# Performance work log

Measured on AMD Instinct MI355X. Metric: run time of the kernel, lower is better.

The kernel has to match this reference:

```python
import jax, jax.numpy as jnp
import numpy as np

N_A, N_P, E = 50000, 50000, 600000
H, D = 8, 16
C = H * D  # hidden_channels = 128
OUT = 16
F_A, F_P = 256, 128
NEG_SLOPE = 0.2
EPS = 1e-5


def setup_inputs():
    key = jax.random.key(0)
    ks = jax.random.split(key, 16)
    return {
        'x_author': jax.random.normal(ks[0], (N_A, F_A), jnp.float32),
        'x_paper': jax.random.normal(ks[1], (N_P, F_P), jnp.float32),
        'W_a': jax.random.normal(ks[2], (F_A, C), jnp.float32) / np.sqrt(F_A).astype(np.float32),
        'b_a': jnp.zeros((C,), jnp.float32),
        'W_p': jax.random.normal(ks[3], (F_P, C), jnp.float32) / np.sqrt(F_P).astype(np.float32),
        'b_p': jnp.zeros((C,), jnp.float32),
        'att_src_ap': jax.random.normal(ks[4], (H, D), jnp.float32) * 0.1,
        'att_dst_ap': jax.random.normal(ks[5], (H, D), jnp.float32) * 0.1,
        'att_src_pp': jax.random.normal(ks[6], (H, D), jnp.float32) * 0.1,
        'att_dst_pp': jax.random.normal(ks[7], (H, D), jnp.float32) * 0.1,
        'k_W': jax.random.normal(ks[8], (C, C), jnp.float32) / np.sqrt(C).astype(np.float32),
        'k_b': jnp.zeros((C,), jnp.float32),
        'q': jax.random.normal(ks[9], (C,), jnp.float32) * 0.1,
        'norm_w': jnp.ones((C,), jnp.float32),
        'norm_b': jnp.zeros((C,), jnp.float32),
        'norm_ms': jnp.ones((C,), jnp.float32),
        'lin_W': jax.random.normal(ks[10], (C, OUT), jnp.float32) / np.sqrt(C).astype(np.float32),
        'lin_b': jnp.zeros((OUT,), jnp.float32),
        'edge_ap': jax.random.randint(ks[11], (2, E), 0, N_A),
        'edge_pp': jax.random.randint(ks[12], (2, E), 0, N_P),
    }


def _edge_type_out(h_src, h_dst, edge, a_src, a_dst, n_dst):
    # Node-level attention for one edge type (PyG HANConv per-metapath GAT).
    alpha_s = jnp.einsum('nhd,hd->nh', h_src, a_src)  # [N_src, H]
    alpha_d = jnp.einsum('nhd,hd->nh', h_dst, a_dst)  # [N_dst, H]
    src, dst = edge[0], edge[1]
    alpha = alpha_s[src] + alpha_d[dst]                       # [E, H]
    alpha = jnp.where(alpha >= 0, alpha, NEG_SLOPE * alpha)   # leaky_relu(0.2)
    m = jax.ops.segment_max(alpha, dst, num_segments=n_dst)
    e = jnp.exp(alpha - m[dst])
    denom = jax.ops.segment_sum(e, dst, num_segments=n_dst)
    attn = e / denom[dst]                                     # softmax over incoming edges
    msg = h_src[src] * attn[:, :, None]                       # [E, H, D]
    out = jax.ops.segment_sum(msg, dst, num_segments=n_dst)   # [n_dst, H, D]
    return jax.nn.relu(out.reshape(n_dst, H * D))


def reference(x_author, x_paper, W_a, b_a, W_p, b_p, att_src_ap, att_dst_ap,
              att_src_pp, att_dst_pp, k_W, k_b, q, norm_w, norm_b, norm_ms,
              lin_W, lin_b, edge_ap, edge_pp):
    # per-node-type projections -> [N, H, D]
    h_a = (x_author @ W_a + b_a).reshape(N_A, H, D)
    h_p = (x_paper @ W_p + b_p).reshape(N_P, H, D)
    # per-edge-type node-level attention + aggregation (both target 'paper')
    out_ap = _edge_type_out(h_a, h_p, edge_ap, att_src_ap, att_dst_ap, N_P)
    out_pp = _edge_type_out(h_p, h_p, edge_pp, att_src_pp, att_dst_pp, N_P)
    # semantic-level attention across the R=2 meta-paths
    outs = jnp.stack([out_ap, out_pp], axis=0)               # [R, N_P, C]
    w = jnp.tanh(outs @ k_W + k_b).mean(axis=1) @ q          # [R]
    beta = jax.nn.softmax(w)
    out = jnp.einsum('rnc,r->nc', outs, beta)                # [N_P, C]
    # GraphNorm (single graph: stats over all nodes)
    mean = out.mean(axis=0)
    o = out - mean * norm_ms
    var = (o * o).mean(axis=0)
    o = norm_w * o / jnp.sqrt(var + EPS) + norm_b
    # final classifier
    return o @ lin_W + lin_b
```

## Files before the change

### kernel.cpp

```cpp
#include <hip/hip_runtime.h>
#include <math.h>

#define NN   50000
#define EE   600000
#define CCH  128
#define HH   8
#define DD   16
#define OUTC 16
#define NEG  0.2f
#define EPSN 1e-5f
#define SCHUNKS 1172
#define CAP 64
#define SBKT 32

typedef _Float16 f16x8 __attribute__((ext_vector_type(8)));
typedef float    f32x4 __attribute__((ext_vector_type(4)));

__device__ __forceinline__ float fast_tanh(float x) {
    x = fminf(10.f, fmaxf(-10.f, x));
    float e = __expf(2.f * x);
    return (e - 1.f) / (e + 1.f);
}

__device__ __forceinline__ float lrelu(float x) {
    return (x >= 0.f) ? x : NEG * x;
}

__global__ __launch_bounds__(256) void convw_k(const float* __restrict__ W_a,
        const float* __restrict__ W_p, const float* __restrict__ k_W,
        const float* __restrict__ lin_W, _Float16* __restrict__ Wt_a,
        _Float16* __restrict__ Wt_p, _Float16* __restrict__ kWt,
        _Float16* __restrict__ linWt)
{
    int id = blockIdx.x * 256 + threadIdx.x;
    if (id < 32768) {
        int k = id >> 7, n = id & 127;
        Wt_a[n * 256 + k] = (_Float16)W_a[id];
    } else if (id < 49152) {
        int i = id - 32768; int k = i >> 7, n = i & 127;
        Wt_p[n * 128 + k] = (_Float16)W_p[i];
    } else if (id < 65536) {
        int i = id - 49152; int k = i >> 7, n = i & 127;
        kWt[n * 128 + k] = (_Float16)k_W[i];
    } else if (id < 67584) {
        int i = id - 65536; int k = i >> 4, n = i & 15;
        linWt[n * 128 + k] = (_Float16)lin_W[i];
    }
}

__global__ __launch_bounds__(256) void gemm2h_k(const float* __restrict__ X_a,
        const float* __restrict__ X_p, const _Float16* __restrict__ Wt_a,
        const _Float16* __restrict__ Wt_p, const float* __restrict__ b_a,
        const float* __restrict__ b_p,
        const float* __restrict__ att_s_ap, const float* __restrict__ att_d_ap,
        const float* __restrict__ att_s_pp, const float* __restrict__ att_d_pp,
        _Float16* __restrict__ h_a, _Float16* __restrict__ h_p,
        float* __restrict__ as_ap, float* __restrict__ ad_ap,
        float* __restrict__ as_pp, float* __restrict__ ad_pp,
        const int* __restrict__ ea, const int* __restrict__ ep,
        int* __restrict__ fill, int* __restrict__ csrp, int GBn)
{
    __shared__ _Float16 As[64][40];
    __shared__ _Float16 Bs[128][40];
    const int t = threadIdx.x;
    if ((int)blockIdx.x >= 2 * GBn) {
        int bb = (int)blockIdx.x - 2 * GBn;
        int base = bb * 1024 + t;
        int d[4];
#pragma unroll
        for (int it = 0; it < 4; ++it) {
            int e = base + it * 256;
            int dd = -1;
            if (e < EE) dd = ea[EE + e];
            else if (e < 2 * EE) dd = NN + ep[e];
            d[it] = dd;
        }
#pragma unroll
        for (int it = 0; it < 4; ++it) {
            int dd = d[it];
            if (dd >= 0) {
                int e = base + it * 256;
                int pos = atomicAdd(&fill[dd], 1);
                if (pos < CAP) {
                    int s = (e < EE) ? ea[e] : ep[e - EE];
                    csrp[(size_t)dd * CAP + pos] = s;
                }
            }
        }
        return;
    }
    const int which = ((int)blockIdx.x >= GBn) ? 1 : 0;
    const float* X = which ? X_p : X_a;
    const _Float16* Wt = which ? Wt_p : Wt_a;
    const float* bias = which ? b_p : b_a;
    _Float16* Y = which ? h_p : h_a;
    const int K = which ? 128 : 256;
    const int r0 = (blockIdx.x - which * GBn) * 64;
    const int lane = t & 63;
    const int wv = t >> 6;
    const int m16 = lane & 15;
    const int kq = lane >> 4;
    f32x4 acc[8];
#pragma unroll
    for (int i = 0; i < 8; ++i) acc[i] = (f32x4){0.f, 0.f, 0.f, 0.f};

    const int ar = t >> 2;
    const int ak = (t & 3) * 8;
    const int br = t >> 1;
    const int bk = (t & 1) * 16;

    for (int kc = 0; kc < K; kc += 32) {
        int row = r0 + ar;
        f16x8 av;
        if (row < NN) {
            const float4* gp = (const float4*)&X[row * K + kc + ak];
            float4 x0 = gp[0], x1 = gp[1];
            av[0] = (_Float16)x0.x; av[1] = (_Float16)x0.y;
            av[2] = (_Float16)x0.z; av[3] = (_Float16)x0.w;
            av[4] = (_Float16)x1.x; av[5] = (_Float16)x1.y;
            av[6] = (_Float16)x1.z; av[7] = (_Float16)x1.w;
        } else {
#pragma unroll
            for (int j = 0; j < 8; ++j) av[j] = (_Float16)0.f;
        }
        *(f16x8*)&As[ar][ak] = av;
        const f16x8* wp = (const f16x8*)&Wt[br * K + kc + bk];
        *(f16x8*)&Bs[br][bk]     = wp[0];
        *(f16x8*)&Bs[br][bk + 8] = wp[1];
        __syncthreads();
        f16x8 af = *(const f16x8*)&As[wv * 16 + m16][kq * 8];
#pragma unroll
        for (int i = 0; i < 8; ++i) {
            f16x8 bf = *(const f16x8*)&Bs[i * 16 + m16][kq * 8];
            acc[i] = __builtin_amdgcn_mfma_f32_16x16x32_f16(af, bf, acc[i], 0, 0, 0);
        }
        __syncthreads();
    }
    const int rbase = r0 + wv * 16 + kq * 4;
#pragma unroll
    for (int i = 0; i < 8; ++i) {
        int col = i * 16 + m16;
        float bv = bias[col];
        float hv[4];
#pragma unroll
        for (int rr = 0; rr < 4; ++rr) hv[rr] = acc[i][rr] + bv;
#pragma unroll
        for (int rr = 0; rr < 4; ++rr)
            if (rbase + rr < NN) Y[(rbase + rr) * 128 + col] = (_Float16)hv[rr];
        if (which == 0) {
            float av = att_s_ap[i * 16 + m16];
            float p[4];
#pragma unroll
            for (int rr = 0; rr < 4; ++rr) p[rr] = hv[rr] * av;
#pragma unroll
            for (int x = 1; x < 16; x <<= 1)
#pragma unroll
                for (int rr = 0; rr < 4; ++rr) p[rr] += __shfl_xor(p[rr], x, 64);
            if (m16 == 0) {
#pragma unroll
                for (int rr = 0; rr < 4; ++rr)
                    if (rbase + rr < NN) as_ap[(rbase + rr) * 8 + i] = p[rr];
            }
        } else {
            float a1 = att_d_ap[i * 16 + m16];
            float a2 = att_s_pp[i * 16 + m16];
            float a3 = att_d_pp[i * 16 + m16];
            float p1[4], p2[4], p3[4];
#pragma unroll
            for (int rr = 0; rr < 4; ++rr) {
                p1[rr] = hv[rr] * a1; p2[rr] = hv[rr] * a2; p3[rr] = hv[rr] * a3;
            }
#pragma unroll
            for (int x = 1; x < 16; x <<= 1) {
#pragma unroll
                for (int rr = 0; rr < 4; ++rr) {
                    p1[rr] += __shfl_xor(p1[rr], x, 64);
                    p2[rr] += __shfl_xor(p2[rr], x, 64);
                    p3[rr] += __shfl_xor(p3[rr], x, 64);
                }
            }
            if (m16 == 0) {
#pragma unroll
                for (int rr = 0; rr < 4; ++rr) {
                    if (rbase + rr < NN) {
                        ad_ap[(rbase + rr) * 8 + i] = p1[rr];
                        as_pp[(rbase + rr) * 8 + i] = p2[rr];
                        ad_pp[(rbase + rr) * 8 + i] = p3[rr];
                    }
                }
            }
        }
    }
}

__device__ __forceinline__ void agg_path(
        const _Float16* __restrict__ hsrc, const float* __restrict__ as,
        float adv, int cnt, const int* __restrict__ row, int h, int sub,
        float* acc, float& l)
{
    int4 r0 = *(const int4*)&row[0];
    int4 r1 = *(const int4*)&row[4];
    int4 r2 = *(const int4*)&row[8];
    int4 r3 = *(const int4*)&row[12];
    int s[16] = {r0.x, r0.y, r0.z, r0.w, r1.x, r1.y, r1.z, r1.w,
                 r2.x, r2.y, r2.z, r2.w, r3.x, r3.y, r3.z, r3.w};
#pragma unroll
    for (int e = 0; e < 16; ++e) s[e] = (e < cnt) ? s[e] : 0;
    float av[16];
#pragma unroll
    for (int e = 0; e < 16; ++e) av[e] = as[s[e] * 8 + h];
    f16x8 hv[16];
#pragma unroll
    for (int e = 0; e < 16; ++e)
        hv[e] = *(const f16x8*)&hsrc[(size_t)s[e] * CCH + sub * 8];
#pragma unroll
    for (int e = 0; e < 16; ++e) {
        float w = (e < cnt) ? __expf(lrelu(av[e] + adv)) : 0.f;
        l += w;
#pragma unroll
        for (int i = 0; i < 8; ++i) acc[i] += w * (float)hv[e][i];
    }
    if (cnt > 16) {
        int4 r4 = *(const int4*)&row[16];
        int4 r5 = *(const int4*)&row[20];
        int s2[8] = {r4.x, r4.y, r4.z, r4.w, r5.x, r5.y, r5.z, r5.w};
#pragma unroll
        for (int e = 0; e < 8; ++e) s2[e] = (16 + e < cnt) ? s2[e] : 0;
        float av2[8];
#pragma unroll
        for (int e = 0; e < 8; ++e) av2[e] = as[s2[e] * 8 + h];
        f16x8 hv2[8];
#pragma unroll
        for (int e = 0; e < 8; ++e)
            hv2[e] = *(const f16x8*)&hsrc[(size_t)s2[e] * CCH + sub * 8];
#pragma unroll
        for (int e = 0; e < 8; ++e) {
            float w = (16 + e < cnt) ? __expf(lrelu(av2[e] + adv)) : 0.f;
            l += w;
#pragma unroll
            for (int i = 0; i < 8; ++i) acc[i] += w * (float)hv2[e][i];
        }
        for (int p = 24; p < cnt; ++p) {
            int s0 = row[p];
            float w = __expf(lrelu(as[s0 * 8 + h] + adv));
            f16x8 v = *(const f16x8*)&hsrc[(size_t)s0 * CCH + sub * 8];
            l += w;
#pragma unroll
            for (int i = 0; i < 8; ++i) acc[i] += w * (float)v[i];
        }
    }
}

__global__ __launch_bounds__(256) void agg4f_k(
        const _Float16* __restrict__ h_a, const _Float16* __restrict__ h_p,
        const float* __restrict__ as_ap, const float* __restrict__ ad_ap,
        const float* __restrict__ as_pp, const float* __restrict__ ad_pp,
        const int* __restrict__ fill, const int* __restrict__ csrp,
        const _Float16* __restrict__ kWt, const float* __restrict__ kb,
        const float* __restrict__ qv,
        _Float16* __restrict__ out_ap, _Float16* __restrict__ out_pp,
        float* __restrict__ wacc, float* __restrict__ statsb)
{
    __shared__ _Float16 Aap[16][136];
    __shared__ _Float16 App[16][136];
    __shared__ float sbuf[640];
    __shared__ float wred[4];
    const int t = threadIdx.x;
    const int wave = t >> 6, lane = t & 63;
    const int q = lane >> 4, sub = lane & 15;
    const int slot = wave * 4 + q;
    const int n = blockIdx.x * 16 + slot;
    const int h = sub >> 1;
    for (int i = t; i < 640; i += 256) sbuf[i] = 0.f;

    float adva = ad_ap[n * 8 + h];
    float advp = ad_pp[n * 8 + h];
    int cnt_a = fill[n];      if (cnt_a > CAP) cnt_a = CAP;
    int cnt_p = fill[NN + n]; if (cnt_p > CAP) cnt_p = CAP;
    float la = 0.f, lp = 0.f;
    float accA[8] = {0.f,0.f,0.f,0.f,0.f,0.f,0.f,0.f};
    float accP[8] = {0.f,0.f,0.f,0.f,0.f,0.f,0.f,0.f};

    agg_path(h_a, as_ap, adva, cnt_a, &csrp[(size_t)n * CAP],        h, sub, accA, la);
    agg_path(h_p, as_pp, advp, cnt_p, &csrp[(size_t)(NN + n) * CAP], h, sub, accP, lp);

    float inva = (la > 0.f) ? 1.f/la : 0.f;
    float invp = (lp > 0.f) ? 1.f/lp : 0.f;
    float oa[8], ob[8];
#pragma unroll
    for (int i = 0; i < 8; ++i) {
        oa[i] = fmaxf(accA[i]*inva, 0.f);
        ob[i] = fmaxf(accP[i]*invp, 0.f);
    }
    f16x8 va, vb;
#pragma unroll
    for (int i = 0; i < 8; ++i) { va[i] = (_Float16)oa[i]; vb[i] = (_Float16)ob[i]; }
    *(f16x8*)&out_ap[n * CCH + sub * 8] = va;
    *(f16x8*)&out_pp[n * CCH + sub * 8] = vb;
    *(f16x8*)&Aap[slot][sub * 8] = va;
    *(f16x8*)&App[slot][sub * 8] = vb;
    float sa[8], sb[8], ssa[8], ssb[8], sab[8];
#pragma unroll
    for (int j = 0; j < 8; ++j) {
        float a = oa[j], bq = ob[j];
        sa[j] = a; sb[j] = bq; ssa[j] = a*a; ssb[j] = bq*bq; sab[j] = a*bq;
    }
#pragma unroll
    for (int x = 16; x < 64; x <<= 1) {
#pragma unroll
        for (int j = 0; j < 8; ++j) {
            sa[j]  += __shfl_xor(sa[j],  x, 64);
            sb[j]  += __shfl_xor(sb[j],  x, 64);
            ssa[j] += __shfl_xor(ssa[j], x, 64);
            ssb[j] += __shfl_xor(ssb[j], x, 64);
            sab[j] += __shfl_xor(sab[j], x, 64);
        }
    }
    __syncthreads();
    if (lane < 16) {
        int c0 = sub * 8;
#pragma unroll
        for (int j = 0; j < 8; ++j) {
            atomicAdd(&sbuf[c0 + j],       sa[j]);
            atomicAdd(&sbuf[128 + c0 + j], sb[j]);
            atomicAdd(&sbuf[256 + c0 + j], ssa[j]);
            atomicAdd(&sbuf[384 + c0 + j], ssb[j]);
            atomicAdd(&sbuf[512 + c0 + j], sab[j]);
        }
    }
    const int m16 = lane & 15, kq = lane >> 4;
    const int path = wave >> 1;
    float local = 0.f;
#pragma unroll
    for (int j = 0; j < 4; ++j) {
        int ct = (wave & 1) * 4 + j;
        f32x4 acc2 = (f32x4){0.f, 0.f, 0.f, 0.f};
#pragma unroll
        for (int kc = 0; kc < 128; kc += 32) {
            f16x8 af = path ? *(const f16x8*)&App[m16][kc + kq * 8]
                            : *(const f16x8*)&Aap[m16][kc + kq * 8];
            f16x8 bf = *(const f16x8*)&kWt[(ct * 16 + m16) * 128 + kc + kq * 8];
            acc2 = __builtin_amdgcn_mfma_f32_16x16x32_f16(af, bf, acc2, 0, 0, 0);
        }
        float kbc = kb[ct * 16 + m16], qc = qv[ct * 16 + m16];
#pragma unroll
        for (int rr = 0; rr < 4; ++rr)
            local += fast_tanh(acc2[rr] + kbc) * qc;
    }
#pragma unroll
    for (int x = 1; x < 64; x <<= 1) local += __shfl_xor(local, x, 64);
    if (lane == 0) wred[wave] = local;
    __syncthreads();
    if (t == 0) atomicAdd(&wacc[(blockIdx.x & 15) * 16],       wred[0] + wred[1]);
    if (t == 1) atomicAdd(&wacc[256 + (blockIdx.x & 15) * 16], wred[2] + wred[3]);
    if (t < 128) {
        float* sp = statsb + (size_t)(blockIdx.x & (SBKT - 1)) * 128;
        atomicAdd(&sp[t],                sbuf[t]);
        atomicAdd(&sp[SBKT*128 + t],     sbuf[128 + t]);
        atomicAdd(&sp[2*SBKT*128 + t],   sbuf[256 + t]);
        atomicAdd(&sp[3*SBKT*128 + t],   sbuf[384 + t]);
        atomicAdd(&sp[4*SBKT*128 + t],   sbuf[512 + t]);
    }
}

__global__ __launch_bounds__(256) void final2_k(
        const _Float16* __restrict__ oa, const _Float16* __restrict__ ob,
        const float* __restrict__ wacc, const float* __restrict__ statsb,
        const float* __restrict__ ms, const float* __restrict__ nw,
        const float* __restrict__ nb,
        const _Float16* __restrict__ linWt, const float* __restrict__ linb,
        float* __restrict__ out)
{
    __shared__ _Float16 As[64][136];
    __shared__ float scl[128], shf[128];
    __shared__ float bcoef[2];
    int t = threadIdx.x;
    if (t < 128) {
        float w0s = 0.f, w1s = 0.f;
#pragma unroll
        for (int i = 0; i < 16; ++i) {
            w0s += wacc[i * 16];
            w1s += wacc[256 + i * 16];
        }
        float w0 = w0s * (1.f / NN), w1 = w1s * (1.f / NN);
        float mm = fmaxf(w0, w1);
        float e0 = __expf(w0 - mm), e1 = __expf(w1 - mm);
        float b0 = e0 / (e0 + e1), b1 = e1 / (e0 + e1);
        if (t == 0) { bcoef[0] = b0; bcoef[1] = b1; }
        int c = t;
        float vsA = 0.f, vsB = 0.f, vssA = 0.f, vssB = 0.f, vsAB = 0.f;
        for (int i = 0; i < SBKT; ++i) {
            vsA  += statsb[i * 128 + c];
            vsB  += statsb[SBKT*128 + i * 128 + c];
            vssA += statsb[2*SBKT*128 + i * 128 + c];
            vssB += statsb[3*SBKT*128 + i * 128 + c];
            vsAB += statsb[4*SBKT*128 + i * 128 + c];
        }
        float mean = (b0 * vsA + b1 * vsB) * (1.f / NN);
        float ex2 = (b0 * b0 * vssA + 2.f * b0 * b1 * vsAB + b1 * b1 * vssB) * (1.f / NN);
        float a = mean * ms[c];
        float var = ex2 - 2.f * a * mean + a * a;
        float sc = nw[c] * rsqrtf(var + EPSN);
        scl[c] = sc;
        shf[c] = nb[c] - a * sc;
    }
    __syncthreads();
    float b0 = bcoef[0], b1 = bcoef[1];
    int r0 = blockIdx.x * 64;
    int row = t >> 2, cp = (t & 3) * 32;
    int gr = r0 + row;
    if (gr < NN) {
#pragma unroll
        for (int i = 0; i < 4; ++i) {
            int c0 = cp + i * 8;
            f16x8 va = *(const f16x8*)&oa[gr * CCH + c0];
            f16x8 vb = *(const f16x8*)&ob[gr * CCH + c0];
            f16x8 o;
#pragma unroll
            for (int e2 = 0; e2 < 8; ++e2) {
                float v = b0 * (float)va[e2] + b1 * (float)vb[e2];
                o[e2] = (_Float16)(v * scl[c0 + e2] + shf[c0 + e2]);
            }
            *(f16x8*)&As[row][c0] = o;
        }
    } else {
        f16x8 z;
#pragma unroll
        for (int e2 = 0; e2 < 8; ++e2) z[e2] = (_Float16)0.f;
#pragma unroll
        for (int i = 0; i < 4; ++i) *(f16x8*)&As[row][cp + i * 8] = z;
    }
    __syncthreads();
    int lane = t & 63, wv = t >> 6;
    int m16 = lane & 15, kq = lane >> 4;
    f32x4 acc = (f32x4){0.f, 0.f, 0.f, 0.f};
#pragma unroll
    for (int kc = 0; kc < 128; kc += 32) {
        f16x8 af = *(const f16x8*)&As[wv * 16 + m16][kc + kq * 8];
        f16x8 bf = *(const f16x8*)&linWt[m16 * 128 + kc + kq * 8];
        acc = __builtin_amdgcn_mfma_f32_16x16x32_f16(af, bf, acc, 0, 0, 0);
    }
    float lb = linb[m16];
#pragma unroll
    for (int r = 0; r < 4; ++r) {
        int gr2 = r0 + wv * 16 + kq * 4 + r;
        if (gr2 < NN) out[gr2 * 16 + m16] = acc[r] + lb;
    }
}

extern "C" void kernel_launch(void* const* d_in, const int* in_sizes, int n_in,
                              void* d_out, int out_size, void* d_ws, size_t ws_size,
                              hipStream_t stream) {
    const float* x_a   = (const float*)d_in[0];
    const float* x_p   = (const float*)d_in[1];
    const float* W_a   = (const float*)d_in[2];
    const float* b_a   = (const float*)d_in[3];
    const float* W_p   = (const float*)d_in[4];
    const float* b_p   = (const float*)d_in[5];
    const float* att_src_ap = (const float*)d_in[6];
    const float* att_dst_ap = (const float*)d_in[7];
    const float* att_src_pp = (const float*)d_in[8];
    const float* att_dst_pp = (const float*)d_in[9];
    const float* k_W   = (const float*)d_in[10];
    const float* k_b   = (const float*)d_in[11];
    const float* q     = (const float*)d_in[12];
    const float* norm_w = (const float*)d_in[13];
    const float* norm_b = (const float*)d_in[14];
    const float* norm_ms = (const float*)d_in[15];
    const float* lin_W = (const float*)d_in[16];
    const float* lin_b = (const float*)d_in[17];
    const int* edge_ap = (const int*)d_in[18];
    const int* edge_pp = (const int*)d_in[19];
    float* out = (float*)d_out;

    char* base = (char*)d_ws;
    size_t off = 0;
    auto alloc = [&](size_t bytes) -> void* {
        void* r = base + off;
        off += (bytes + 255) & ~(size_t)255;
        return r;
    };
    _Float16* h_a    = (_Float16*)alloc((size_t)NN * CCH * 2);
    _Float16* h_p    = (_Float16*)alloc((size_t)NN * CCH * 2);
    _Float16* out_ap = (_Float16*)alloc((size_t)NN * CCH * 2);
    _Float16* out_pp = (_Float16*)alloc((size_t)NN * CCH * 2);
    float* as_ap  = (float*)alloc((size_t)NN * HH * 4);
    float* ad_ap  = (float*)alloc((size_t)NN * HH * 4);
    float* as_pp  = (float*)alloc((size_t)NN * HH * 4);
    float* ad_pp  = (float*)alloc((size_t)NN * HH * 4);
    _Float16* Wt_a = (_Float16*)alloc((size_t)128 * 256 * 2);
    _Float16* Wt_p = (_Float16*)alloc((size_t)128 * 128 * 2);
    _Float16* kWt  = (_Float16*)alloc((size_t)128 * 128 * 2);
    _Float16* linWt = (_Float16*)alloc((size_t)16 * 128 * 2);
    int* csrp = (int*)alloc((size_t)2 * NN * CAP * 4);
    const size_t ZCOUNT = 100000 + 512 + 5 * SBKT * 128;
    int* zz = (int*)alloc(ZCOUNT * 4);
    int* fill   = zz;
    float* wacc = (float*)(zz + 100000);
    float* statsb = (float*)(zz + 100512);

    (void)in_sizes; (void)n_in; (void)out_size; (void)ws_size;

    hipMemsetAsync(zz, 0, ZCOUNT * 4, stream);

    convw_k<<<264, 256, 0, stream>>>(W_a, W_p, k_W, lin_W, Wt_a, Wt_p, kWt, linWt);

    const int GB = (NN + 63) / 64;
    gemm2h_k<<<2 * GB + SCHUNKS, 256, 0, stream>>>(
        x_a, x_p, Wt_a, Wt_p, b_a, b_p,
        att_src_ap, att_dst_ap, att_src_pp, att_dst_pp,
        h_a, h_p, as_ap, ad_ap, as_pp, ad_pp,
        edge_ap, edge_pp, fill, csrp, GB);

    agg4f_k<<<NN / 16, 256, 0, stream>>>(h_a, h_p, as_ap, ad_ap, as_pp, ad_pp,
                                         fill, csrp, kWt, k_b, q,
                                         out_ap, out_pp, wacc, statsb);

    final2_k<<<GB, 256, 0, stream>>>(out_ap, out_pp, wacc, statsb,
                                     norm_ms, norm_w, norm_b, linWt, lin_b, out);
}
```

Measured before the change: 334.0 us.

## Split aggregation waves per metapath, store attention logits in fp16, simplify stats

The aggregation kernel now gives each wave one metapath for 8 nodes per block, instead of having every wave walk both metapaths for 16 nodes. This doubles the grid and halves the serial gather work per thread, which should expose more memory-level parallelism. The per-node attention logits are stored as fp16 to cut gather bytes. GraphNorm statistics are now summed from the shared tiles by 128 threads, replacing the shuffle and shared-atomic reductions. The cost is zero-padded MFMA rows that do wasted work, fp16 rounding of the attention logits, and twice as many global atomics.

```diff
diff --git a/kernel.cpp b/kernel.cpp
--- a/kernel.cpp
+++ b/kernel.cpp
@@ -55,8 +55,8 @@
         const float* __restrict__ att_s_ap, const float* __restrict__ att_d_ap,
         const float* __restrict__ att_s_pp, const float* __restrict__ att_d_pp,
         _Float16* __restrict__ h_a, _Float16* __restrict__ h_p,
-        float* __restrict__ as_ap, float* __restrict__ ad_ap,
-        float* __restrict__ as_pp, float* __restrict__ ad_pp,
+        _Float16* __restrict__ as_ap, _Float16* __restrict__ ad_ap,
+        _Float16* __restrict__ as_pp, _Float16* __restrict__ ad_pp,
         const int* __restrict__ ea, const int* __restrict__ ep,
         int* __restrict__ fill, int* __restrict__ csrp, int GBn)
 {
@@ -159,7 +159,7 @@
             if (m16 == 0) {
 #pragma unroll
                 for (int rr = 0; rr < 4; ++rr)
-                    if (rbase + rr < NN) as_ap[(rbase + rr) * 8 + i] = p[rr];
+                    if (rbase + rr < NN) as_ap[(rbase + rr) * 8 + i] = (_Float16)p[rr];
             }
         } else {
             float a1 = att_d_ap[i * 16 + m16];
@@ -183,9 +183,9 @@
 #pragma unroll
                 for (int rr = 0; rr < 4; ++rr) {
                     if (rbase + rr < NN) {
-                        ad_ap[(rbase + rr) * 8 + i] = p1[rr];
-                        as_pp[(rbase + rr) * 8 + i] = p2[rr];
-                        ad_pp[(rbase + rr) * 8 + i] = p3[rr];
+                        ad_ap[(rbase + rr) * 8 + i] = (_Float16)p1[rr];
+                        as_pp[(rbase + rr) * 8 + i] = (_Float16)p2[rr];
+                        ad_pp[(rbase + rr) * 8 + i] = (_Float16)p3[rr];
                     }
                 }
             }
@@ -194,7 +194,7 @@
 }
 
 __device__ __forceinline__ void agg_path(
-        const _Float16* __restrict__ hsrc, const float* __restrict__ as,
+        const _Float16* __restrict__ hsrc, const _Float16* __restrict__ as,
         float adv, int cnt, const int* __restrict__ row, int h, int sub,
         float* acc, float& l)
 {
@@ -208,7 +208,7 @@
     for (int e = 0; e < 16; ++e) s[e] = (e < cnt) ? s[e] : 0;
     float av[16];
 #pragma unroll
-    for (int e = 0; e < 16; ++e) av[e] = as[s[e] * 8 + h];
+    for (int e = 0; e < 16; ++e) av[e] = (float)as[s[e] * 8 + h];
     f16x8 hv[16];
 #pragma unroll
     for (int e = 0; e < 16; ++e)
@@ -228,7 +228,7 @@
         for (int e = 0; e < 8; ++e) s2[e] = (16 + e < cnt) ? s2[e] : 0;
         float av2[8];
 #pragma unroll
-        for (int e = 0; e < 8; ++e) av2[e] = as[s2[e] * 8 + h];
+        for (int e = 0; e < 8; ++e) av2[e] = (float)as[s2[e] * 8 + h];
         f16x8 hv2[8];
 #pragma unroll
         for (int e = 0; e < 8; ++e)
@@ -242,7 +242,7 @@
         }
         for (int p = 24; p < cnt; ++p) {
             int s0 = row[p];
-            float w = __expf(lrelu(as[s0 * 8 + h] + adv));
+            float w = __expf(lrelu((float)as[s0 * 8 + h] + adv));
             f16x8 v = *(const f16x8*)&hsrc[(size_t)s0 * CCH + sub * 8];
             l += w;
 #pragma unroll
@@ -253,8 +253,8 @@
 
 __global__ __launch_bounds__(256) void agg4f_k(
         const _Float16* __restrict__ h_a, const _Float16* __restrict__ h_p,
-        const float* __restrict__ as_ap, const float* __restrict__ ad_ap,
-        const float* __restrict__ as_pp, const float* __restrict__ ad_pp,
+        const _Float16* __restrict__ as_ap, const _Float16* __restrict__ ad_ap,
+        const _Float16* __restrict__ as_pp, const _Float16* __restrict__ ad_pp,
         const int* __restrict__ fill, const int* __restrict__ csrp,
         const _Float16* __restrict__ kWt, const float* __restrict__ kb,
         const float* __restrict__ qv,
@@ -263,73 +263,46 @@
 {
     __shared__ _Float16 Aap[16][136];
     __shared__ _Float16 App[16][136];
-    __shared__ float sbuf[640];
     __shared__ float wred[4];
     const int t = threadIdx.x;
     const int wave = t >> 6, lane = t & 63;
     const int q = lane >> 4, sub = lane & 15;
-    const int slot = wave * 4 + q;
-    const int n = blockIdx.x * 16 + slot;
+    const int pw = wave >> 1;
+    const int slot = (wave & 1) * 4 + q;
+    const int n = blockIdx.x * 8 + slot;
     const int h = sub >> 1;
-    for (int i = t; i < 640; i += 256) sbuf[i] = 0.f;
-
-    float adva = ad_ap[n * 8 + h];
-    float advp = ad_pp[n * 8 + h];
-    int cnt_a = fill[n];      if (cnt_a > CAP) cnt_a = CAP;
-    int cnt_p = fill[NN + n]; if (cnt_p > CAP) cnt_p = CAP;
-    float la = 0.f, lp = 0.f;
-    float accA[8] = {0.f,0.f,0.f,0.f,0.f,0.f,0.f,0.f};
-    float accP[8] = {0.f,0.f,0.f,0.f,0.f,0.f,0.f,0.f};
-
-    agg_path(h_a, as_ap, adva, cnt_a, &csrp[(size_t)n * CAP],        h, sub, accA, la);
-    agg_path(h_p, as_pp, advp, cnt_p, &csrp[(size_t)(NN + n) * CAP], h, sub, accP, lp);
-
-    float inva = (la > 0.f) ? 1.f/la : 0.f;
-    float invp = (lp > 0.f) ? 1.f/lp : 0.f;
-    float oa[8], ob[8];
-#pragma unroll
-    for (int i = 0; i < 8; ++i) {
-        oa[i] = fmaxf(accA[i]*inva, 0.f);
-        ob[i] = fmaxf(accP[i]*invp, 0.f);
-    }
-    f16x8 va, vb;
-#pragma unroll
-    for (int i = 0; i < 8; ++i) { va[i] = (_Float16)oa[i]; vb[i] = (_Float16)ob[i]; }
-    *(f16x8*)&out_ap[n * CCH + sub * 8] = va;
-    *(f16x8*)&out_pp[n * CCH + sub * 8] = vb;
-    *(f16x8*)&Aap[slot][sub * 8] = va;
-    *(f16x8*)&App[slot][sub * 8] = vb;
-    float sa[8], sb[8], ssa[8], ssb[8], sab[8];
-#pragma unroll
-    for (int j = 0; j < 8; ++j) {
-        float a = oa[j], bq = ob[j];
-        sa[j] = a; sb[j] = bq; ssa[j] = a*a; ssb[j] = bq*bq; sab[j] = a*bq;
-    }
-#pragma unroll
-    for (int x = 16; x < 64; x <<= 1) {
-#pragma unroll
-        for (int j = 0; j < 8; ++j) {
-            sa[j]  += __shfl_xor(sa[j],  x, 64);
-            sb[j]  += __shfl_xor(sb[j],  x, 64);
-            ssa[j] += __shfl_xor(ssa[j], x, 64);
-            ssb[j] += __shfl_xor(ssb[j], x, 64);
-            sab[j] += __shfl_xor(sab[j], x, 64);
-        }
+    {
+        _Float16* za = &Aap[8][0];
+        _Float16* zb = &App[8][0];
+        for (int i = t; i < 8 * 136; i += 256) {
+            za[i] = (_Float16)0.f; zb[i] = (_Float16)0.f;
+        }
+    }
+    const _Float16* hsrc = pw ? h_p : h_a;
+    const _Float16* as   = pw ? as_pp : as_ap;
+    const _Float16* ad   = pw ? ad_pp : ad_ap;
+    const int gnode = pw ? NN + n : n;
+    float adv = (float)ad[n * 8 + h];
+    int cnt = fill[gnode]; if (cnt > CAP) cnt = CAP;
+    const int* row = &csrp[(size_t)gnode * CAP];
+    float l = 0.f;
+    float acc[8] = {0.f,0.f,0.f,0.f,0.f,0.f,0.f,0.f};
+
+    agg_path(hsrc, as, adv, cnt, row, h, sub, acc, l);
+
+    float inv = (l > 0.f) ? 1.f / l : 0.f;
+    f16x8 vo;
+#pragma unroll
+    for (int i = 0; i < 8; ++i) vo[i] = (_Float16)fmaxf(acc[i] * inv, 0.f);
+    if (pw == 0) {
+        *(f16x8*)&out_ap[n * CCH + sub * 8] = vo;
+        *(f16x8*)&Aap[slot][sub * 8] = vo;
+    } else {
+        *(f16x8*)&out_pp[n * CCH + sub * 8] = vo;
+        *(f16x8*)&App[slot][sub * 8] = vo;
     }
     __syncthreads();
-    if (lane < 16) {
-        int c0 = sub * 8;
-#pragma unroll
-        for (int j = 0; j < 8; ++j) {
-            atomicAdd(&sbuf[c0 + j],       sa[j]);
-            atomicAdd(&sbuf[128 + c0 + j], sb[j]);
-            atomicAdd(&sbuf[256 + c0 + j], ssa[j]);
-            atomicAdd(&sbuf[384 + c0 + j], ssb[j]);
-            atomicAdd(&sbuf[512 + c0 + j], sab[j]);
-        }
-    }
     const int m16 = lane & 15, kq = lane >> 4;
-    const int path = wave >> 1;
     float local = 0.f;
 #pragma unroll
     for (int j = 0; j < 4; ++j) {
@@ -337,15 +310,17 @@
         f32x4 acc2 = (f32x4){0.f, 0.f, 0.f, 0.f};
 #pragma unroll
         for (int kc = 0; kc < 128; kc += 32) {
-            f16x8 af = path ? *(const f16x8*)&App[m16][kc + kq * 8]
-                            : *(const f16x8*)&Aap[m16][kc + kq * 8];
+            f16x8 af = pw ? *(const f16x8*)&App[m16][kc + kq * 8]
+                          : *(const f16x8*)&Aap[m16][kc + kq * 8];
             f16x8 bf = *(const f16x8*)&kWt[(ct * 16 + m16) * 128 + kc + kq * 8];
             acc2 = __builtin_amdgcn_mfma_f32_16x16x32_f16(af, bf, acc2, 0, 0, 0);
         }
-        float kbc = kb[ct * 16 + m16], qc = qv[ct * 16 + m16];
-#pragma unroll
-        for (int rr = 0; rr < 4; ++rr)
-            local += fast_tanh(acc2[rr] + kbc) * qc;
+        if (kq < 2) {
+            float kbc = kb[ct * 16 + m16], qc = qv[ct * 16 + m16];
+#pragma unroll
+            for (int rr = 0; rr < 4; ++rr)
+                local += fast_tanh(acc2[rr] + kbc) * qc;
+        }
     }
 #pragma unroll
     for (int x = 1; x < 64; x <<= 1) local += __shfl_xor(local, x, 64);
@@ -354,12 +329,20 @@
     if (t == 0) atomicAdd(&wacc[(blockIdx.x & 15) * 16],       wred[0] + wred[1]);
     if (t == 1) atomicAdd(&wacc[256 + (blockIdx.x & 15) * 16], wred[2] + wred[3]);
     if (t < 128) {
+        int c = t;
+        float vsa = 0.f, vsb = 0.f, vssa = 0.f, vssb = 0.f, vsab = 0.f;
+#pragma unroll
+        for (int r = 0; r < 8; ++r) {
+            float a = (float)Aap[r][c];
+            float b = (float)App[r][c];
+            vsa += a; vsb += b; vssa += a * a; vssb += b * b; vsab += a * b;
+        }
         float* sp = statsb + (size_t)(blockIdx.x & (SBKT - 1)) * 128;
-        atomicAdd(&sp[t],                sbuf[t]);
-        atomicAdd(&sp[SBKT*128 + t],     sbuf[128 + t]);
-        atomicAdd(&sp[2*SBKT*128 + t],   sbuf[256 + t]);
-        atomicAdd(&sp[3*SBKT*128 + t],   sbuf[384 + t]);
-        atomicAdd(&sp[4*SBKT*128 + t],   sbuf[512 + t]);
+        atomicAdd(&sp[c],                vsa);
+        atomicAdd(&sp[SBKT*128 + c],     vsb);
+        atomicAdd(&sp[2*SBKT*128 + c],   vssa);
+        atomicAdd(&sp[3*SBKT*128 + c],   vssb);
+        atomicAdd(&sp[4*SBKT*128 + c],   vsab);
     }
 }
 
@@ -484,10 +467,10 @@
     _Float16* h_p    = (_Float16*)alloc((size_t)NN * CCH * 2);
     _Float16* out_ap = (_Float16*)alloc((size_t)NN * CCH * 2);
     _Float16* out_pp = (_Float16*)alloc((size_t)NN * CCH * 2);
-    float* as_ap  = (float*)alloc((size_t)NN * HH * 4);
-    float* ad_ap  = (float*)alloc((size_t)NN * HH * 4);
-    float* as_pp  = (float*)alloc((size_t)NN * HH * 4);
-    float* ad_pp  = (float*)alloc((size_t)NN * HH * 4);
+    _Float16* as_ap  = (_Float16*)alloc((size_t)NN * HH * 2);
+    _Float16* ad_ap  = (_Float16*)alloc((size_t)NN * HH * 2);
+    _Float16* as_pp  = (_Float16*)alloc((size_t)NN * HH * 2);
+    _Float16* ad_pp  = (_Float16*)alloc((size_t)NN * HH * 2);
     _Float16* Wt_a = (_Float16*)alloc((size_t)128 * 256 * 2);
     _Float16* Wt_p = (_Float16*)alloc((size_t)128 * 128 * 2);
     _Float16* kWt  = (_Float16*)alloc((size_t)128 * 128 * 2);
@@ -512,9 +495,9 @@
         h_a, h_p, as_ap, ad_ap, as_pp, ad_pp,
         edge_ap, edge_pp, fill, csrp, GB);
 
-    agg4f_k<<<NN / 16, 256, 0, stream>>>(h_a, h_p, as_ap, ad_ap, as_pp, ad_pp,
-                                         fill, csrp, kWt, k_b, q,
-                                         out_ap, out_pp, wacc, statsb);
+    agg4f_k<<<NN / 8, 256, 0, stream>>>(h_a, h_p, as_ap, ad_ap, as_pp, ad_pp,
+                                        fill, csrp, kWt, k_b, q,
+                                        out_ap, out_pp, wacc, statsb);
 
     final2_k<<<GB, 256, 0, stream>>>(out_ap, out_pp, wacc, statsb,
                                      norm_ms, norm_w, norm_b, linWt, lin_b, out);
```

After: 337.0 us. Within noise of the previous version (+0.9%).
